# Performance work log

Measured on AMD Instinct MI355X. Metric: run time of the kernel, lower is better.

Reference implementation:

```python
import jax, jax.numpy as jnp
import numpy as np

NSIDE = 64
NLAT = 4 * NSIDE - 1        # 255 iso-latitude rings
NLON = 4 * NSIDE            # 256 = max pixels per ring
NPIX = 12 * NSIDE * NSIDE   # 49152 HEALPix pixels
LMAX = NLAT                 # 255
MMAX = NLON // 2 + 1        # 129
BATCH, CHAN = 8, 32


def _ring_geometry():
    # HEALPix ring scheme: ring r (0-based), 1-based i=r+1
    #  north cap i<nside: nph=4i, phi shift 0.5
    #  equatorial nside<=i<=3*nside: nph=4*nside, shift alternates {0,0.5}
    #  south cap: mirror of north cap
    nph = np.zeros(NLAT, np.int64)
    shift = np.zeros(NLAT, np.float64)
    for r in range(NLAT):
        i = r + 1
        if i < NSIDE:
            nph[r], shift[r] = 4 * i, 0.5
        elif i <= 3 * NSIDE:
            nph[r], shift[r] = 4 * NSIDE, 0.5 * ((i - NSIDE + 1) % 2)
        else:
            nph[r], shift[r] = 4 * (NLAT - r), 0.5
    offs = np.concatenate([[0], np.cumsum(nph)[:-1]])
    p = np.arange(NLON)
    mask = (p[None, :] < nph[:, None])                       # [nlat, nlon]
    idx = (offs[:, None] + p[None, :]) * mask                # padded -> 0
    phase = 2.0 * np.pi * (p[None, :] + shift[:, None]) / nph[:, None] * mask
    return idx.astype(np.int32), mask.astype(np.float32), phase.astype(np.float32)


def setup_inputs() -> dict:
    key = jax.random.key(0)
    k1, k2, k3 = jax.random.split(key, 3)
    idx, mask, phase = _ring_geometry()
    x = jax.random.normal(k1, (BATCH, CHAN, NPIX), jnp.float32)
    pct = jax.random.normal(k2, (MMAX, LMAX, NLAT), jnp.float32) * 0.1  # Legendre table stand-in
    w = jax.random.uniform(k3, (NLAT,), jnp.float32)                    # per-ring quadrature weights
    return {"x": x, "pct": pct, "w": w,
            "ring_index": jnp.asarray(idx),
            "ring_mask": jnp.asarray(mask),
            "phase": jnp.asarray(phase)}


def _healpix_rfft_real(x, ring_index, ring_mask, phase):
    # x: [..., npix] -> per-ring DFT coefficients as real pairs [..., nlat, mmax, 2]
    rings = x[..., ring_index] * ring_mask                 # [..., nlat, nlon]
    m = jnp.arange(MMAX, dtype=phase.dtype)
    ang = phase[:, :, None] * m                            # [nlat, nlon, mmax]
    fr = jnp.einsum('...kp,kpm->...km', rings, jnp.cos(ang))
    fi = -jnp.einsum('...kp,kpm->...km', rings, jnp.sin(ang))
    return jnp.stack([fr, fi], axis=-1)                    # n=2 is view_as_real axis


def reference(x, pct, w, ring_index, ring_mask, phase):
    # healpix ring rFFT, then Legendre contraction (einsum '...kmn,mlk->...lmn')
    f = _healpix_rfft_real(x, ring_index, ring_mask, phase)  # [..., nlat, mmax, 2]
    weights = pct * w                                        # [mmax, lmax, nlat]
    out = jnp.einsum('...kmn,mlk->...lmn', f, weights)       # [..., lmax, mmax, 2]
    return out
```

## Files before the change

kernel.cpp:

```cpp
#include <hip/hip_runtime.h>

#define NLAT 255
#define NLON 256
#define NPIX 49152
#define MMAX 129
#define MCS  258
#define NTBL 65
#define TROWS 264

typedef unsigned short ushort_t;
typedef __attribute__((ext_vector_type(8)))  short  bf16x8;
typedef __attribute__((ext_vector_type(4)))  short  short4v;
typedef __attribute__((ext_vector_type(16))) float  f32x16;
typedef __attribute__((ext_vector_type(4)))  float  float4v;

__device__ __forceinline__ ushort_t f2bf(float f) {
    union { float f; unsigned u; } v; v.f = f;
    unsigned r = v.u + 0x7FFFu + ((v.u >> 16) & 1u);
    return (ushort_t)(r >> 16);
}
__device__ __forceinline__ float bf2f(ushort_t h) {
    union { unsigned u; float f; } v; v.u = ((unsigned)h) << 16;
    return v.f;
}

__global__ __launch_bounds__(256) void prepK(const float* __restrict__ pct,
                                             const float* __restrict__ w,
                                             ushort_t* __restrict__ pctwF) {
    const int m  = blockIdx.x;
    const int l0 = blockIdx.y * 32;
    const int t  = threadIdx.x;
    const float wk = (t < NLAT) ? w[t] : 0.f;
    const int kg = t >> 3, j = t & 7;
    for (int l = l0; l < l0 + 32; ++l) {
        float v = 0.f;
        if (l < NLAT && t < NLAT)
            v = pct[((size_t)m * NLAT + l) * NLAT + t] * wk;
        pctwF[(((size_t)m * 32 + kg) * 256 + l) * 8 + j] = f2bf(v);
    }
}

__global__ __launch_bounds__(256) void trigK(const float* __restrict__ phase,
                                             const float* __restrict__ mask,
                                             ushort_t* __restrict__ Ttab3) {
    const int tt  = blockIdx.x;
    const int mcs = blockIdx.y;
    const int p   = threadIdx.x;
    const int r   = (tt < 63) ? tt : (tt == 63 ? 63 : 64);
    float val = 0.f;
    if (mcs < MCS) {
        float ph = phase[r * NLON + p];
        float mk = mask[r * NLON + p];
        float fm = (float)(mcs >> 1);
        float s, c;
        __sincosf(ph * fm, &s, &c);
        val = (mcs & 1) ? (-s * mk) : (c * mk);
    }
    const int pcc = p >> 6, c = (p >> 3) & 7, j = p & 7;
    Ttab3[((((size_t)tt * 4 + pcc) * 8 + c) * TROWS + mcs) * 8 + j] = f2bf(val);
}

__global__ __launch_bounds__(256, 2) void stageA(const float* __restrict__ x,
                                                 const int* __restrict__ ring_index,
                                                 const ushort_t* __restrict__ Ttab3,
                                                 ushort_t* __restrict__ f1) {
    __shared__ __align__(16) ushort_t Rs[2][64 * 72];

    const int b0 = blockIdx.x * 64;
    const int r  = blockIdx.y;
    const int i1 = r + 1;
    const int nph = (i1 < 64) ? 4 * i1 : (i1 <= 192 ? 256 : 4 * (256 - i1));
    const int tbl = (i1 < 64) ? r : (i1 <= 192 ? (63 + (((i1 - 63) & 1) ^ 1)) : 254 - r);
    const int base = ring_index[r * NLON];
    const int nchunks = (nph + 63) >> 6;

    const int t    = threadIdx.x;
    const int lane = t & 63;
    const int wid  = t >> 6;
    const int wrow = wid >> 1, wcol = wid & 1;
    const int lg   = lane >> 5;
    const int lc   = lane & 31;

    f32x16 acc[5];
#pragma unroll
    for (int tau = 0; tau < 5; ++tau)
#pragma unroll
        for (int q = 0; q < 16; ++q) acc[tau][q] = 0.f;

    int trow[5];
#pragma unroll
    for (int tau = 0; tau < 5; ++tau) {
        int rr = tau * 64 + wcol * 32 + lc;
        trow[tau] = rr > (TROWS - 1) ? (TROWS - 1) : rr;
    }

    float4v rx[4];
    const int p0 = (t & 15) * 4;
    auto ldX = [&](int pc) {
        const bool ok = (pc + p0) < nph;
#pragma unroll
        for (int pass = 0; pass < 4; ++pass) {
            int bc = (t >> 4) + pass * 16;
            float4v v = {0.f, 0.f, 0.f, 0.f};
            if (ok) v = *(const float4v*)(x + (size_t)(b0 + bc) * NPIX + base + pc + p0);
            rx[pass] = v;
        }
    };
    auto stX = [&](ushort_t* dst) {
#pragma unroll
        for (int pass = 0; pass < 4; ++pass) {
            int bc = (t >> 4) + pass * 16;
            short4v h;
            h[0] = (short)f2bf(rx[pass][0]); h[1] = (short)f2bf(rx[pass][1]);
            h[2] = (short)f2bf(rx[pass][2]); h[3] = (short)f2bf(rx[pass][3]);
            *(short4v*)(dst + bc * 72 + p0) = h;
        }
    };

    ldX(0);
    stX(Rs[0]);
    __syncthreads();

    for (int c = 0; c < nchunks; ++c) {
        const int pc = c << 6;
        const bool more = (c + 1) < nchunks;
        const ushort_t* slab = Ttab3 + (size_t)(tbl * 4 + c) * (8 * TROWS * 8);

        bf16x8 bfr[4][5];
#pragma unroll
        for (int ks = 0; ks < 4; ++ks) {
            const ushort_t* bcol = slab + (size_t)(ks * 2 + lg) * (TROWS * 8);
#pragma unroll
            for (int tau = 0; tau < 5; ++tau)
                bfr[ks][tau] = *(const bf16x8*)(bcol + trow[tau] * 8);
        }
        if (more) ldX(pc + 64);

        const ushort_t* Rcur = Rs[c & 1];
#pragma unroll
        for (int ks = 0; ks < 4; ++ks) {
            bf16x8 a = *(const bf16x8*)(Rcur + (wrow * 32 + lc) * 72 + ks * 16 + lg * 8);
#pragma unroll
            for (int tau = 0; tau < 5; ++tau)
                acc[tau] = __builtin_amdgcn_mfma_f32_32x32x16_bf16(a, bfr[ks][tau], acc[tau], 0, 0, 0);
        }
        if (more) stX(Rs[(c + 1) & 1]);
        __syncthreads();
    }

    ushort_t* Olds = Rs[0];
#pragma unroll
    for (int tau = 0; tau < 5; ++tau) {
        __syncthreads();
        {
            const int mcsl = wcol * 32 + lc;
#pragma unroll
            for (int q = 0; q < 16; ++q) {
                int bcl = wrow * 32 + 4 * lg + (q & 3) + 8 * (q >> 2);
                Olds[mcsl * 72 + bcl] = f2bf(acc[tau][q]);
            }
        }
        __syncthreads();
        {
            int row = t >> 2;
            int mcs = tau * 64 + row;
            if (mcs < MCS) {
                int m = mcs >> 1, n = mcs & 1;
                size_t gbase = ((size_t)m * NLAT + r) * 512 + n * 256 + b0 + (t & 3) * 16;
#pragma unroll
                for (int j = 0; j < 2; ++j) {
                    bf16x8 v = *(const bf16x8*)(Olds + row * 72 + (t & 3) * 16 + j * 8);
                    *(bf16x8*)(f1 + gbase + j * 8) = v;
                }
            }
        }
    }
}

__global__ __launch_bounds__(256) void transK(const ushort_t* __restrict__ f1,
                                              ushort_t* __restrict__ f1tF) {
    __shared__ __align__(16) ushort_t T[64][72];
    const int m  = blockIdx.x;
    const int k0 = blockIdx.y * 64;
    const int b0 = blockIdx.z * 64;
    const int t  = threadIdx.x;
#pragma unroll
    for (int it = 0; it < 2; ++it) {
        int id = t + it * 256;
        int kk = id >> 3, ch = id & 7;
        int k  = k0 + kk;
        bf16x8 v = {0,0,0,0,0,0,0,0};
        if (k < NLAT)
            v = *(const bf16x8*)(f1 + ((size_t)m * NLAT + k) * 512 + b0 + ch * 8);
        *(bf16x8*)(&T[kk][ch * 8]) = v;
    }
    __syncthreads();
#pragma unroll
    for (int it = 0; it < 2; ++it) {
        int id  = t + it * 256;
        int bb  = id & 63, ch8 = id >> 6;
        bf16x8 v;
#pragma unroll
        for (int j = 0; j < 8; ++j) v[j] = T[ch8 * 8 + j][bb];
        *(bf16x8*)(f1tF + (((size_t)m * 32 + (k0 >> 3) + ch8) * 512 + b0 + bb) * 8) = v;
    }
}

__global__ __launch_bounds__(256, 3) void stageB(const ushort_t* __restrict__ f1tF,
                                                 const ushort_t* __restrict__ pctwF,
                                                 ushort_t* __restrict__ otmp) {
    __shared__ __align__(16) ushort_t SB[24576];
    ushort_t* Es = SB;

    const int id = blockIdx.x;
    const int m  = ((id >> 5) << 3) | (id & 7);
    if (m >= MMAX) return;
    const int b2t = ((id >> 3) & 3) * 128;

    const int t    = threadIdx.x;
    const int lane = t & 63;
    const int wid  = t >> 6;
    const int wrow = wid >> 1, wlcol = wid & 1;
    const int lg   = lane >> 5, lc = lane & 31;

    f32x16 acc[2][4];
#pragma unroll
    for (int i = 0; i < 2; ++i)
#pragma unroll
        for (int j = 0; j < 4; ++j)
#pragma unroll
            for (int q = 0; q < 16; ++q) acc[i][j][q] = 0.f;

    const ushort_t* aSrc = f1tF  + (size_t)m * 32 * 512 * 8;
    const ushort_t* wSrc = pctwF + (size_t)m * 32 * 256 * 8;

    auto STAGE = [&](int buf, int c) {
#pragma unroll
        for (int u = 0; u < 2; ++u) {
            int sA   = wid * 2 + u;
            int kg   = c * 4 + (sA >> 1);
            int half = sA & 1;
            const ushort_t* src = aSrc + ((size_t)kg * 512 + b2t + half * 64) * 8 + lane * 8;
            __builtin_amdgcn_global_load_lds(
                (const __attribute__((address_space(1))) void*)src,
                (__attribute__((address_space(3))) void*)(SB + buf * 4096 + sA * 512),
                16, 0, 0);
        }
#pragma unroll
        for (int u = 0; u < 4; ++u) {
            int sW = wid * 4 + u;
            int kg = c * 4 + (sW >> 2);
            int q  = sW & 3;
            const ushort_t* src = wSrc + ((size_t)kg * 256 + q * 64) * 8 + lane * 8;
            __builtin_amdgcn_global_load_lds(
                (const __attribute__((address_space(1))) void*)src,
                (__attribute__((address_space(3))) void*)(SB + 8192 + buf * 8192 + sW * 512),
                16, 0, 0);
        }
    };

    STAGE(0, 0);
    __syncthreads();
    int buf = 0;
    for (int c = 0; c < 8; ++c, buf ^= 1) {
        if (c + 1 < 8) STAGE(buf ^ 1, c + 1);
        const ushort_t* A = SB + buf * 4096;
        const ushort_t* W = SB + 8192 + buf * 8192;
#pragma unroll
        for (int ks = 0; ks < 2; ++ks) {
            const int kgl = ks * 2 + lg;
            bf16x8 a0 = *(const bf16x8*)(A + (kgl * 128 + wrow * 64 + lc) * 8);
            bf16x8 a1 = *(const bf16x8*)(A + (kgl * 128 + wrow * 64 + 32 + lc) * 8);
#pragma unroll
            for (int jj = 0; jj < 4; ++jj) {
                bf16x8 b = *(const bf16x8*)(W + (kgl * 256 + wlcol * 128 + jj * 32 + lc) * 8);
                acc[0][jj] = __builtin_amdgcn_mfma_f32_32x32x16_bf16(a0, b, acc[0][jj], 0, 0, 0);
                acc[1][jj] = __builtin_amdgcn_mfma_f32_32x32x16_bf16(a1, b, acc[1][jj], 0, 0, 0);
            }
        }
        __syncthreads();
    }

#pragma unroll
    for (int h = 0; h < 2; ++h) {
        if (h) __syncthreads();
        if (wlcol == h) {
#pragma unroll
            for (int i = 0; i < 2; ++i)
#pragma unroll
                for (int jj = 0; jj < 4; ++jj)
#pragma unroll
                    for (int q = 0; q < 16; ++q) {
                        int bl = wrow * 64 + i * 32 + 4 * lg + (q & 3) + 8 * (q >> 2);
                        Es[bl * 136 + jj * 32 + lc] = f2bf(acc[i][jj][q]);
                    }
        }
        __syncthreads();
#pragma unroll
        for (int it = 0; it < 8; ++it) {
            int id2 = t + it * 256;
            int row = id2 >> 4, ch = id2 & 15;
            bf16x8 v = *(const bf16x8*)(Es + row * 136 + ch * 8);
            *(bf16x8*)(otmp + (((size_t)m * 512 + b2t + row) << 8) + h * 128 + ch * 8) = v;
        }
    }
}

__global__ __launch_bounds__(256) void permuteK(const ushort_t* __restrict__ otmp,
                                                float* __restrict__ out) {
    __shared__ ushort_t L[MCS * 66];
    const int bc = blockIdx.x;
    const int l0 = blockIdx.y * 64;
    const int t  = threadIdx.x;
    const int ll = t & 63;
    const int l  = l0 + ll;
#pragma unroll 4
    for (int it = 0; it < 65; ++it) {
        int mn = (t >> 6) + it * 4;
        if (mn < MCS) {
            int mm = mn >> 1, n = mn & 1;
            ushort_t v = 0;
            if (l < NLAT)
                v = otmp[(((size_t)mm * 512 + n * 256 + bc) << 8) + l];
            L[mn * 66 + ll] = v;
        }
    }
    __syncthreads();
    for (int ll2 = 0; ll2 < 64; ++ll2) {
        int lo = l0 + ll2;
        if (lo >= NLAT) break;
        size_t rowb = ((size_t)bc * NLAT + lo) * MCS;
        out[rowb + t] = bf2f(L[t * 66 + ll2]);
        if (t < 2)
            out[rowb + 256 + t] = bf2f(L[(256 + t) * 66 + ll2]);
    }
}

extern "C" void kernel_launch(void* const* d_in, const int* in_sizes, int n_in,
                              void* d_out, int out_size, void* d_ws, size_t ws_size,
                              hipStream_t stream) {
    const float* x          = (const float*)d_in[0];
    const float* pct        = (const float*)d_in[1];
    const float* w          = (const float*)d_in[2];
    const int*   ring_index = (const int*)d_in[3];
    const float* ring_mask  = (const float*)d_in[4];
    const float* phase      = (const float*)d_in[5];
    float* out = (float*)d_out;

    char* wsb = (char*)d_ws;
    char* ob  = (char*)d_out;
    ushort_t* otmp  = (ushort_t*)wsb;
    ushort_t* f1    = (ushort_t*)(wsb + 33552384);
    ushort_t* f1tF  = (ushort_t*)ob;
    ushort_t* pctwF = (ushort_t*)(ob + 33816576);
    ushort_t* Ttab3 = (ushort_t*)(ob + 50724864);

    prepK   <<<dim3(MMAX, 8),     256, 0, stream>>>(pct, w, pctwF);
    trigK   <<<dim3(NTBL, TROWS), 256, 0, stream>>>(phase, ring_mask, Ttab3);
    stageA  <<<dim3(4, NLAT),     256, 0, stream>>>(x, ring_index, Ttab3, f1);
    transK  <<<dim3(MMAX, 4, 8),  256, 0, stream>>>(f1, f1tF);
    stageB  <<<dim3(544),         256, 0, stream>>>(f1tF, pctwF, otmp);
    permuteK<<<dim3(256, 4),      256, 0, stream>>>(otmp, out);
}
```

Before: 118.8 us.

## Stage whole ring of x into LDS upfront with XOR swizzle, drop per-chunk barriers

Replaces the double-buffered per-chunk load/convert pipeline with a single prologue that loads all ring chunks of x into a 64x256 bf16 LDS tile, using an XOR swizzle on 8-element groups to avoid bank conflicts. The MFMA loop then runs with no barriers between chunks. This removes per-chunk __syncthreads but gives up overlap of global loads with MFMA work, and raises LDS use to 32KB per block, which may limit occupancy relative to launch_bounds(256,2).

```diff
diff --git a/kernel.cpp b/kernel.cpp
--- a/kernel.cpp
+++ b/kernel.cpp
@@ -64,7 +64,7 @@
                                                  const int* __restrict__ ring_index,
                                                  const ushort_t* __restrict__ Ttab3,
                                                  ushort_t* __restrict__ f1) {
-    __shared__ __align__(16) ushort_t Rs[2][64 * 72];
+    __shared__ __align__(16) ushort_t Rs[64 * 256];
 
     const int b0 = blockIdx.x * 64;
     const int r  = blockIdx.y;
@@ -94,37 +94,31 @@
         trow[tau] = rr > (TROWS - 1) ? (TROWS - 1) : rr;
     }
 
-    float4v rx[4];
-    const int p0 = (t & 15) * 4;
-    auto ldX = [&](int pc) {
-        const bool ok = (pc + p0) < nph;
-#pragma unroll
-        for (int pass = 0; pass < 4; ++pass) {
-            int bc = (t >> 4) + pass * 16;
-            float4v v = {0.f, 0.f, 0.f, 0.f};
-            if (ok) v = *(const float4v*)(x + (size_t)(b0 + bc) * NPIX + base + pc + p0);
-            rx[pass] = v;
-        }
-    };
-    auto stX = [&](ushort_t* dst) {
-#pragma unroll
-        for (int pass = 0; pass < 4; ++pass) {
-            int bc = (t >> 4) + pass * 16;
-            short4v h;
-            h[0] = (short)f2bf(rx[pass][0]); h[1] = (short)f2bf(rx[pass][1]);
-            h[2] = (short)f2bf(rx[pass][2]); h[3] = (short)f2bf(rx[pass][3]);
-            *(short4v*)(dst + bc * 72 + p0) = h;
-        }
-    };
-
-    ldX(0);
-    stX(Rs[0]);
+    {
+        const int p0  = (t & 15) * 4;
+        const int c16 = p0 >> 3;
+        const int hf  = (p0 >> 2) & 1;
+        for (int cc = 0; cc < nchunks; ++cc) {
+            const int pc = cc << 6;
+            const bool ok = (pc + p0) < nph;
+#pragma unroll
+            for (int pass = 0; pass < 4; ++pass) {
+                int bc = (t >> 4) + pass * 16;
+                float4v v = {0.f, 0.f, 0.f, 0.f};
+                if (ok) v = *(const float4v*)(x + (size_t)(b0 + bc) * NPIX + base + pc + p0);
+                short4v h;
+                h[0] = (short)f2bf(v[0]); h[1] = (short)f2bf(v[1]);
+                h[2] = (short)f2bf(v[2]); h[3] = (short)f2bf(v[3]);
+                int dst = bc * 256 + cc * 64 + ((c16 ^ (bc & 7)) << 3) + (hf << 2);
+                *(short4v*)(Rs + dst) = h;
+            }
+        }
+    }
     __syncthreads();
 
-    for (int c = 0; c < nchunks; ++c) {
-        const int pc = c << 6;
-        const bool more = (c + 1) < nchunks;
-        const ushort_t* slab = Ttab3 + (size_t)(tbl * 4 + c) * (8 * TROWS * 8);
+    const int arow = wrow * 32 + lc;
+    for (int cc = 0; cc < nchunks; ++cc) {
+        const ushort_t* slab = Ttab3 + (size_t)(tbl * 4 + cc) * (8 * TROWS * 8);
 
         bf16x8 bfr[4][5];
 #pragma unroll
@@ -134,21 +128,17 @@
             for (int tau = 0; tau < 5; ++tau)
                 bfr[ks][tau] = *(const bf16x8*)(bcol + trow[tau] * 8);
         }
-        if (more) ldX(pc + 64);
-
-        const ushort_t* Rcur = Rs[c & 1];
 #pragma unroll
         for (int ks = 0; ks < 4; ++ks) {
-            bf16x8 a = *(const bf16x8*)(Rcur + (wrow * 32 + lc) * 72 + ks * 16 + lg * 8);
+            bf16x8 a = *(const bf16x8*)(Rs + arow * 256 + cc * 64 +
+                                        (((ks * 2 + lg) ^ (arow & 7)) << 3));
 #pragma unroll
             for (int tau = 0; tau < 5; ++tau)
                 acc[tau] = __builtin_amdgcn_mfma_f32_32x32x16_bf16(a, bfr[ks][tau], acc[tau], 0, 0, 0);
         }
-        if (more) stX(Rs[(c + 1) & 1]);
-        __syncthreads();
-    }
-
-    ushort_t* Olds = Rs[0];
+    }
+
+    ushort_t* Olds = Rs;
 #pragma unroll
     for (int tau = 0; tau < 5; ++tau) {
         __syncthreads();
```

New measurement: 131.4 us. +10.6%, slower.
